# Kernel optimization log

Hardware: AMD Instinct MI355X
Metric: run time of the kernel (lower is better)

## Reference

```python
import jax, jax.numpy as jnp
import numpy as np

B, N, S, D_IN, D_OUT = 8, 8192, 8, 64, 64


def setup_inputs() -> dict:
    key = jax.random.key(0)
    ks = jax.random.split(key, 7)
    x = jax.random.normal(ks[0], (B, N, D_IN), dtype=jnp.float32)
    j_idx = jax.random.randint(ks[1], (B, N, S), 0, N, dtype=jnp.int32)
    k_idx = jax.random.randint(ks[2], (B, N, S), 0, N, dtype=jnp.int32)
    # MLP params: Linear(3d -> 2d), GELU, Linear(2d -> d_out)
    s1 = 1.0 / np.sqrt(3 * D_IN)
    s2 = 1.0 / np.sqrt(2 * D_IN)
    W1 = jax.random.uniform(ks[3], (3 * D_IN, 2 * D_IN), jnp.float32, -s1, s1)
    b1 = jax.random.uniform(ks[4], (2 * D_IN,), jnp.float32, -s1, s1)
    W2 = jax.random.uniform(ks[5], (2 * D_IN, D_OUT), jnp.float32, -s2, s2)
    b2 = jax.random.uniform(ks[6], (D_OUT,), jnp.float32, -s2, s2)
    return {"x": x, "j_idx": j_idx, "k_idx": k_idx, "W1": W1, "b1": b1, "W2": W2, "b2": b2}


def reference(x, j_idx, k_idx, W1, b1, W2, b2):
    # x: (B,N,D); j_idx/k_idx: (B,N,S) indices into N
    gather = jax.vmap(lambda xb, ib: xb[ib])  # per-batch gather -> (N,S,D)
    xj = gather(x, j_idx)                      # (B,N,S,D)
    xk = gather(x, k_idx)                      # (B,N,S,D)
    xi = jnp.broadcast_to(x[:, :, None, :], xj.shape)
    triple = jnp.concatenate([xi, xj, xk], axis=-1)  # (B,N,S,3D)
    h = jax.nn.gelu(triple @ W1 + b1, approximate=False)  # (B,N,S,2D)
    out = h @ W2 + b2                                       # (B,N,S,D_OUT)
    return out.mean(axis=2)                                 # (B,N,D_OUT)
```

## Files before the change

kernel.cpp:

```cpp
#include <hip/hip_runtime.h>
#include <stdint.h>


#define NT   8
#define NBLK 2048

typedef short  short8 __attribute__((ext_vector_type(8)));
typedef float  f32x4  __attribute__((ext_vector_type(4)));
typedef float  f32x16 __attribute__((ext_vector_type(16)));

__device__ __forceinline__ unsigned short f2bf(float f){
  union { float f; unsigned u; } a; a.f = f;
  unsigned u = a.u;
  u += 0x7fffu + ((u >> 16) & 1u);
  return (unsigned short)(u >> 16);
}
__device__ __forceinline__ float fast_gelu(float x){
  float x2 = x * x;
  float t  = __builtin_fmaf(x2, -0.1029437f, -2.3022083f);
  float p  = __builtin_amdgcn_exp2f(x * t);
  return x * __builtin_amdgcn_rcpf(1.0f + p);
}

__global__ void prep_kernel(const float* __restrict__ x, const float* __restrict__ W1,
                            const float* __restrict__ W2, short* __restrict__ xb,
                            short* __restrict__ w1f, short* __restrict__ w2f){
  int bid = blockIdx.x;
  if (bid < 2048){
    long i = (long)bid * 256 + threadIdx.x;
    const float4* p = (const float4*)(x + i * 8);
    float4 a = p[0], b = p[1];
    short8 v;
    v[0]=(short)f2bf(a.x); v[1]=(short)f2bf(a.y); v[2]=(short)f2bf(a.z); v[3]=(short)f2bf(a.w);
    v[4]=(short)f2bf(b.x); v[5]=(short)f2bf(b.y); v[6]=(short)f2bf(b.z); v[7]=(short)f2bf(b.w);
    *(short8*)(xb + i * 8) = v;
  } else if (threadIdx.x < 64){
    int f = bid - 2048, lane = threadIdx.x;
    short8 v;
    if (f < 48){
      int cb = f / 12, t = f % 12;
      #pragma unroll
      for (int j = 0; j < 8; j++)
        v[j] = (short)f2bf(W1[(t*16 + 8*(lane>>5) + j)*128 + cb*32 + (lane&31)]);
      *(short8*)(w1f + ((long)(f*64 + lane))*8) = v;
    } else {
      int g = f - 48; int w = g >> 2, q = g & 3;
      #pragma unroll
      for (int j = 0; j < 8; j++)
        v[j] = (short)f2bf(W2[(q*32 + 8*(lane>>4) + j)*64 + w*16 + (lane&15)]);
      *(short8*)(w2f + ((long)(g*64 + lane))*8) = v;
    }
  }
}

__global__ __launch_bounds__(256, 4) void ltc_main(
    const short* __restrict__ xb,  const short* __restrict__ w1f,
    const short* __restrict__ w2f, const int* __restrict__ jidx,
    const int* __restrict__ kidx,  const float* __restrict__ b1,
    const float* __restrict__ b2,  float* __restrict__ out)
{
  __shared__ short Ab[2][4608];
  __shared__ short HB[2][4 * 136];

  const int tid  = threadIdx.x;
  const int w    = tid >> 6, lane = tid & 63;
  const int l31  = lane & 31, hi = lane >> 5;
  const int l15  = lane & 15, q4 = lane >> 4;

  short8 w1v[12];
  #pragma unroll
  for (int t = 0; t < 12; t++)
    w1v[t] = *(const short8*)(w1f + ((long)((w * 12 + t) * 64 + lane)) * 8);
  short8 w2v[4];
  #pragma unroll
  for (int q = 0; q < 4; q++)
    w2v[q] = *(const short8*)(w2f + ((long)((w * 4 + q) * 64 + lane)) * 8);

  float b1v = b1[w * 32 + l31];
  float b2v = b2[w * 16 + l15];

  const int bid   = blockIdx.x;
  const int batch = bid & 7;
  const int tile0 = batch * 2048 + (bid >> 3) * NT;
  const long tb0  = (long)tile0 * 32;
  const int bbase = batch << 13;

  const int o_r = (lane >> 3) & 3;
  const int o_c = (lane & 7) ^ o_r;

  const int rown = l31 >> 3;
  const int oOb  = rown * 128;
  const int oJ   = 1024 + hi * 512 + l31 * 16;
  const int oK   = oJ + 4096;

  auto stage = [&](int buf, long tb, int jn, int kn){
    const short* gj = xb + (long)(bbase + jn) * 64 + (2 * w + hi) * 8;
    __builtin_amdgcn_global_load_lds(
        (const __attribute__((address_space(1))) unsigned int*)gj,
        (__attribute__((address_space(3))) unsigned int*)(&Ab[buf][512 + w * 512]), 16, 0, 0);
    const short* gk = xb + (long)(bbase + kn) * 64 + (2 * w + hi) * 8;
    __builtin_amdgcn_global_load_lds(
        (const __attribute__((address_space(1))) unsigned int*)gk,
        (__attribute__((address_space(3))) unsigned int*)(&Ab[buf][2560 + w * 512]), 16, 0, 0);
    if (w == 0){
      const short* go = xb + (long)((int)(tb >> 3) + o_r) * 64 + o_c * 8;
      __builtin_amdgcn_global_load_lds(
          (const __attribute__((address_space(1))) unsigned int*)go,
          (__attribute__((address_space(3))) unsigned int*)(&Ab[buf][0]), 16, 0, 0);
    }
  };

  auto gemm2_store = [&](int buf, int ttp){
    f32x4 acc2 = {0.f, 0.f, 0.f, 0.f};
    #pragma unroll
    for (int q = 0; q < 4; q++){
      short8 hbf = *(const short8*)((const char*)&HB[buf][0] + (l15 & 3) * 272 + q * 64 + q4 * 16);
      acc2 = __builtin_amdgcn_mfma_f32_16x16x32_bf16(hbf, w2v[q], acc2, 0, 0, 0);
    }
    if (lane < 16){
      long Gn = ((long)(tile0 + ttp)) * 4;
      #pragma unroll
      for (int r = 0; r < 4; r++)
        out[(Gn + r) * 64 + w * 16 + l15] = acc2[r] + b2v;
    }
  };

  int jn0 = jidx[tb0 + l31], kn0 = kidx[tb0 + l31];
  stage(0, tb0, jn0, kn0);
  int jnS = 0, knS = 0;
  if (NT > 1){ jnS = jidx[tb0 + 32 + l31]; knS = kidx[tb0 + 32 + l31]; }

  for (int tt = 0; tt < NT; ++tt){
    const int cur = tt & 1;
    asm volatile("s_waitcnt vmcnt(0) lgkmcnt(0)\n\ts_barrier" ::: "memory");
    if (tt + 1 < NT) stage(cur ^ 1, tb0 + (long)(tt + 1) * 32, jnS, knS);
    if (tt + 2 < NT){
      jnS = jidx[tb0 + (long)(tt + 2) * 32 + l31];
      knS = kidx[tb0 + (long)(tt + 2) * 32 + l31];
    }

    if (tt > 0) gemm2_store(cur ^ 1, tt - 1);

    const char* Abase = (const char*)&Ab[cur][0];
    f32x16 acc;
    #pragma unroll
    for (int r = 0; r < 16; r++) acc[r] = b1v;
    #pragma unroll
    for (int t = 0; t < 12; t++){
      int off;
      if (t < 4)       off = oOb + (((2*t + hi) ^ rown) << 4);
      else if (t < 8)  off = oJ + (t - 4) * 1024;
      else             off = oK + (t - 8) * 1024;
      short8 af = *(const short8*)(Abase + off);
      acc = __builtin_amdgcn_mfma_f32_32x32x16_bf16(af, w1v[t], acc, 0, 0, 0);
    }

    #pragma unroll
    for (int o = 0; o < 4; o++){
      float s0 = fast_gelu(acc[4*o+0]);
      s0 += fast_gelu(acc[4*o+1]);
      s0 += fast_gelu(acc[4*o+2]);
      s0 += fast_gelu(acc[4*o+3]);
      float other = __shfl_xor(s0, 32);
      float hbv = (s0 + other) * 0.125f;
      if (hi == 0)
        HB[cur][o * 136 + w * 32 + l31] = (short)f2bf(hbv);
    }
  }

  asm volatile("s_waitcnt lgkmcnt(0)\n\ts_barrier" ::: "memory");
  gemm2_store((NT - 1) & 1, NT - 1);
}

__global__ void ltc_naive(const float* __restrict__ x, const int* __restrict__ jidx,
                          const int* __restrict__ kidx, const float* __restrict__ W1,
                          const float* __restrict__ b1, const float* __restrict__ W2,
                          const float* __restrict__ b2, float* __restrict__ out)
{
  int gidx = blockIdx.x;
  int b = gidx >> 13;
  __shared__ float trip[8][192];
  __shared__ float hb[128];
  int t = threadIdx.x;
  for (int i = t; i < 8 * 192; i += 128){
    int s = i / 192, c = i - s * 192;
    int v = c >> 6, cc = c & 63;
    int src;
    if (v == 0)      src = gidx & 8191;
    else if (v == 1) src = jidx[gidx * 8 + s];
    else             src = kidx[gidx * 8 + s];
    trip[s][c] = x[((long)(b << 13) + src) * 64 + cc];
  }
  __syncthreads();
  float z[8];
  #pragma unroll
  for (int s = 0; s < 8; s++) z[s] = b1[t];
  for (int k = 0; k < 192; k++){
    float wv = W1[k * 128 + t];
    #pragma unroll
    for (int s = 0; s < 8; s++) z[s] = fmaf(trip[s][k], wv, z[s]);
  }
  float acc = 0.f;
  #pragma unroll
  for (int s = 0; s < 8; s++) acc += fast_gelu(z[s]);
  hb[t] = acc * 0.125f;
  __syncthreads();
  if (t < 64){
    float o = b2[t];
    for (int h = 0; h < 128; h++) o = fmaf(hb[h], W2[h * 64 + t], o);
    out[(long)gidx * 64 + t] = o;
  }
}

extern "C" void kernel_launch(void* const* d_in, const int* in_sizes, int n_in,
                              void* d_out, int out_size, void* d_ws, size_t ws_size,
                              hipStream_t stream) {
  const float* x   = (const float*)d_in[0];
  const int*   jix = (const int*)  d_in[1];
  const int*   kix = (const int*)  d_in[2];
  const float* W1  = (const float*)d_in[3];
  const float* b1  = (const float*)d_in[4];
  const float* W2  = (const float*)d_in[5];
  const float* b2  = (const float*)d_in[6];
  float* out = (float*)d_out;

  const size_t xb_elems  = (size_t)8 * 8192 * 64;
  const size_t w1f_elems = 48 * 64 * 8;
  const size_t w2f_elems = 16 * 64 * 8;
  const size_t need = (xb_elems + w1f_elems + w2f_elems) * sizeof(short);

  if (ws_size >= need){
    short* xb  = (short*)d_ws;
    short* w1f = xb + xb_elems;
    short* w2f = w1f + w1f_elems;
    prep_kernel<<<2112, 256, 0, stream>>>(x, W1, W2, xb, w1f, w2f);
    ltc_main<<<NBLK, 256, 0, stream>>>(xb, w1f, w2f, jix, kix, b1, b2, out);
  } else {
    ltc_naive<<<8 * 8192, 128, 0, stream>>>(x, jix, kix, W1, b1, W2, b2, out);
  }
}
```

Measured before the change: 56.46 us.

## Process 64-row tiles per block with each wave computing two W1 column blocks

The main kernel now handles 64 (node,sample) rows per iteration instead of 32. Waves are split into two row groups, and each wave computes two 32-column W1 output blocks, so every A fragment read from LDS feeds two MFMAs. Own-node rows are loaded straight from global into registers instead of being staged through LDS, and MFMA issue is raised with s_setprio. The grid is halved, and launch bounds drop to 2 blocks per CU to make room for doubled weight registers and larger LDS buffers, which lowers occupancy.

Result: slower. 58.96 us (+4.4%).

```diff
diff --git a/kernel.cpp b/kernel.cpp
--- a/kernel.cpp
+++ b/kernel.cpp
@@ -3,7 +3,7 @@
 
 
 #define NT   8
-#define NBLK 2048
+#define NBLK 1024
 
 typedef short  short8 __attribute__((ext_vector_type(8)));
 typedef float  f32x4  __attribute__((ext_vector_type(4)));
@@ -53,118 +53,141 @@
   }
 }
 
-__global__ __launch_bounds__(256, 4) void ltc_main(
+__global__ __launch_bounds__(256, 2) void ltc_main(
     const short* __restrict__ xb,  const short* __restrict__ w1f,
     const short* __restrict__ w2f, const int* __restrict__ jidx,
     const int* __restrict__ kidx,  const float* __restrict__ b1,
     const float* __restrict__ b2,  float* __restrict__ out)
 {
-  __shared__ short Ab[2][4608];
-  __shared__ short HB[2][4 * 136];
+  __shared__ short Ab[2][8192];
+  __shared__ short HB[2][8 * 136];
 
   const int tid  = threadIdx.x;
   const int w    = tid >> 6, lane = tid & 63;
+  const int tg   = w >> 1, q = w & 1;
   const int l31  = lane & 31, hi = lane >> 5;
   const int l15  = lane & 15, q4 = lane >> 4;
 
-  short8 w1v[12];
-  #pragma unroll
-  for (int t = 0; t < 12; t++)
-    w1v[t] = *(const short8*)(w1f + ((long)((w * 12 + t) * 64 + lane)) * 8);
+  short8 w1a[12], w1b[12];
+  #pragma unroll
+  for (int t = 0; t < 12; t++){
+    w1a[t] = *(const short8*)(w1f + ((long)(((2*q    ) * 12 + t) * 64 + lane)) * 8);
+    w1b[t] = *(const short8*)(w1f + ((long)(((2*q + 1) * 12 + t) * 64 + lane)) * 8);
+  }
   short8 w2v[4];
   #pragma unroll
-  for (int q = 0; q < 4; q++)
-    w2v[q] = *(const short8*)(w2f + ((long)((w * 4 + q) * 64 + lane)) * 8);
-
-  float b1v = b1[w * 32 + l31];
-  float b2v = b2[w * 16 + l15];
+  for (int q2 = 0; q2 < 4; q2++)
+    w2v[q2] = *(const short8*)(w2f + ((long)((w * 4 + q2) * 64 + lane)) * 8);
+
+  const float b1a = b1[(2*q    ) * 32 + l31];
+  const float b1b = b1[(2*q + 1) * 32 + l31];
+  const float b2v = b2[w * 16 + l15];
 
   const int bid   = blockIdx.x;
   const int batch = bid & 7;
-  const int tile0 = batch * 2048 + (bid >> 3) * NT;
-  const long tb0  = (long)tile0 * 32;
+  const int tile0 = batch * 1024 + (bid >> 3) * NT;
+  const long tb0  = (long)tile0 * 64;
   const int bbase = batch << 13;
 
-  const int o_r = (lane >> 3) & 3;
-  const int o_c = (lane & 7) ^ o_r;
-
-  const int rown = l31 >> 3;
-  const int oOb  = rown * 128;
-  const int oJ   = 1024 + hi * 512 + l31 * 16;
-  const int oK   = oJ + 4096;
-
-  auto stage = [&](int buf, long tb, int jn, int kn){
-    const short* gj = xb + (long)(bbase + jn) * 64 + (2 * w + hi) * 8;
-    __builtin_amdgcn_global_load_lds(
-        (const __attribute__((address_space(1))) unsigned int*)gj,
-        (__attribute__((address_space(3))) unsigned int*)(&Ab[buf][512 + w * 512]), 16, 0, 0);
-    const short* gk = xb + (long)(bbase + kn) * 64 + (2 * w + hi) * 8;
-    __builtin_amdgcn_global_load_lds(
-        (const __attribute__((address_space(1))) unsigned int*)gk,
-        (__attribute__((address_space(3))) unsigned int*)(&Ab[buf][2560 + w * 512]), 16, 0, 0);
-    if (w == 0){
-      const short* go = xb + (long)((int)(tb >> 3) + o_r) * 64 + o_c * 8;
+  const int oJ = tg * 8192 + hi * 512 + l31 * 16;
+
+  auto stage = [&](int buf, int jn, int kn){
+    #pragma unroll
+    for (int m = 0; m < 2; m++){
+      const short* gj = xb + (long)(bbase + jn) * 64 + (4*q + 2*m + hi) * 8;
       __builtin_amdgcn_global_load_lds(
-          (const __attribute__((address_space(1))) unsigned int*)go,
-          (__attribute__((address_space(3))) unsigned int*)(&Ab[buf][0]), 16, 0, 0);
+          (const __attribute__((address_space(1))) unsigned int*)gj,
+          (__attribute__((address_space(3))) unsigned int*)(&Ab[buf][tg*4096 + (4*q + 2*m)*256]),
+          16, 0, 0);
+      const short* gk = xb + (long)(bbase + kn) * 64 + (4*q + 2*m + hi) * 8;
+      __builtin_amdgcn_global_load_lds(
+          (const __attribute__((address_space(1))) unsigned int*)gk,
+          (__attribute__((address_space(3))) unsigned int*)(&Ab[buf][tg*4096 + 2048 + (4*q + 2*m)*256]),
+          16, 0, 0);
     }
   };
 
-  auto gemm2_store = [&](int buf, int ttp){
+  auto gemm2_store = [&](int hb, int ttp){
     f32x4 acc2 = {0.f, 0.f, 0.f, 0.f};
     #pragma unroll
-    for (int q = 0; q < 4; q++){
-      short8 hbf = *(const short8*)((const char*)&HB[buf][0] + (l15 & 3) * 272 + q * 64 + q4 * 16);
-      acc2 = __builtin_amdgcn_mfma_f32_16x16x32_bf16(hbf, w2v[q], acc2, 0, 0, 0);
-    }
-    if (lane < 16){
-      long Gn = ((long)(tile0 + ttp)) * 4;
+    for (int q2 = 0; q2 < 4; q2++){
+      short8 hbf = *(const short8*)((const char*)&HB[hb][0] + (l15 & 7) * 272 + q2 * 64 + q4 * 16);
+      acc2 = __builtin_amdgcn_mfma_f32_16x16x32_bf16(hbf, w2v[q2], acc2, 0, 0, 0);
+    }
+    if (lane < 32){
+      long Gn = ((long)(tile0 + ttp)) * 8;
       #pragma unroll
       for (int r = 0; r < 4; r++)
-        out[(Gn + r) * 64 + w * 16 + l15] = acc2[r] + b2v;
+        out[(Gn + 4 * q4 + r) * 64 + w * 16 + l15] = acc2[r] + b2v;
     }
   };
 
-  int jn0 = jidx[tb0 + l31], kn0 = kidx[tb0 + l31];
-  stage(0, tb0, jn0, kn0);
+  int jn = jidx[tb0 + tg * 32 + l31], kn = kidx[tb0 + tg * 32 + l31];
+  stage(0, jn, kn);
   int jnS = 0, knS = 0;
-  if (NT > 1){ jnS = jidx[tb0 + 32 + l31]; knS = kidx[tb0 + 32 + l31]; }
+  if (NT > 1){ jnS = jidx[tb0 + 64 + tg * 32 + l31]; knS = kidx[tb0 + 64 + tg * 32 + l31]; }
 
   for (int tt = 0; tt < NT; ++tt){
     const int cur = tt & 1;
     asm volatile("s_waitcnt vmcnt(0) lgkmcnt(0)\n\ts_barrier" ::: "memory");
-    if (tt + 1 < NT) stage(cur ^ 1, tb0 + (long)(tt + 1) * 32, jnS, knS);
+    if (tt + 1 < NT) stage(cur ^ 1, jnS, knS);
+
+    long tb = tb0 + (long)tt * 64;
+    int own = (int)(tb >> 3) + tg * 4 + (l31 >> 3);
+    short8 afo[4];
+    #pragma unroll
+    for (int t2 = 0; t2 < 4; t2++)
+      afo[t2] = *(const short8*)(xb + (long)own * 64 + (2*t2 + hi) * 8);
+
     if (tt + 2 < NT){
-      jnS = jidx[tb0 + (long)(tt + 2) * 32 + l31];
-      knS = kidx[tb0 + (long)(tt + 2) * 32 + l31];
-    }
-
-    if (tt > 0) gemm2_store(cur ^ 1, tt - 1);
+      jnS = jidx[tb0 + (long)(tt + 2) * 64 + tg * 32 + l31];
+      knS = kidx[tb0 + (long)(tt + 2) * 64 + tg * 32 + l31];
+    }
+
+    if (tt > 0) gemm2_store((tt ^ 1) & 1, tt - 1);
 
     const char* Abase = (const char*)&Ab[cur][0];
-    f32x16 acc;
-    #pragma unroll
-    for (int r = 0; r < 16; r++) acc[r] = b1v;
-    #pragma unroll
-    for (int t = 0; t < 12; t++){
-      int off;
-      if (t < 4)       off = oOb + (((2*t + hi) ^ rown) << 4);
-      else if (t < 8)  off = oJ + (t - 4) * 1024;
-      else             off = oK + (t - 8) * 1024;
-      short8 af = *(const short8*)(Abase + off);
-      acc = __builtin_amdgcn_mfma_f32_32x32x16_bf16(af, w1v[t], acc, 0, 0, 0);
-    }
+    f32x16 accA, accB;
+    #pragma unroll
+    for (int r = 0; r < 16; r++){ accA[r] = b1a; accB[r] = b1b; }
+    __builtin_amdgcn_s_setprio(1);
+    #pragma unroll
+    for (int t = 0; t < 4; t++){
+      accA = __builtin_amdgcn_mfma_f32_32x32x16_bf16(afo[t], w1a[t], accA, 0, 0, 0);
+      accB = __builtin_amdgcn_mfma_f32_32x32x16_bf16(afo[t], w1b[t], accB, 0, 0, 0);
+    }
+    #pragma unroll
+    for (int t = 4; t < 8; t++){
+      short8 af = *(const short8*)(Abase + oJ + (t - 4) * 1024);
+      accA = __builtin_amdgcn_mfma_f32_32x32x16_bf16(af, w1a[t], accA, 0, 0, 0);
+      accB = __builtin_amdgcn_mfma_f32_32x32x16_bf16(af, w1b[t], accB, 0, 0, 0);
+    }
+    #pragma unroll
+    for (int t = 8; t < 12; t++){
+      short8 af = *(const short8*)(Abase + oJ + 4096 + (t - 8) * 1024);
+      accA = __builtin_amdgcn_mfma_f32_32x32x16_bf16(af, w1a[t], accA, 0, 0, 0);
+      accB = __builtin_amdgcn_mfma_f32_32x32x16_bf16(af, w1b[t], accB, 0, 0, 0);
+    }
+    __builtin_amdgcn_s_setprio(0);
 
     #pragma unroll
     for (int o = 0; o < 4; o++){
-      float s0 = fast_gelu(acc[4*o+0]);
-      s0 += fast_gelu(acc[4*o+1]);
-      s0 += fast_gelu(acc[4*o+2]);
-      s0 += fast_gelu(acc[4*o+3]);
-      float other = __shfl_xor(s0, 32);
-      float hbv = (s0 + other) * 0.125f;
-      if (hi == 0)
-        HB[cur][o * 136 + w * 32 + l31] = (short)f2bf(hbv);
+      float sA = fast_gelu(accA[4*o+0]);
+      sA += fast_gelu(accA[4*o+1]);
+      sA += fast_gelu(accA[4*o+2]);
+      sA += fast_gelu(accA[4*o+3]);
+      float sB = fast_gelu(accB[4*o+0]);
+      sB += fast_gelu(accB[4*o+1]);
+      sB += fast_gelu(accB[4*o+2]);
+      sB += fast_gelu(accB[4*o+3]);
+      float oA = __shfl_xor(sA, 32);
+      float oB = __shfl_xor(sB, 32);
+      float hA = (sA + oA) * 0.125f;
+      float hB = (sB + oB) * 0.125f;
+      if (hi == 0){
+        HB[cur][(tg * 4 + o) * 136 + (2*q    ) * 32 + l31] = (short)f2bf(hA);
+        HB[cur][(tg * 4 + o) * 136 + (2*q + 1) * 32 + l31] = (short)f2bf(hB);
+      }
     }
   }
 
```
